# Kernel tuning notes

Measured on AMD Instinct MI355X. Metric: run time of the kernel, lower is better.

The kernel has to match this reference:

```python
import jax, jax.numpy as jnp
import numpy as np

B, C, N = 8, 256, 4096
S = C // 4  # 64
BN_EPS = 1e-5

def setup_inputs() -> dict:
    key = jax.random.key(0)
    ks = jax.random.split(key, 8)
    scale = lambda fan_in: 1.0 / np.sqrt(fan_in)
    x = jax.random.normal(ks[0], (B, C, N), dtype=jnp.float32)
    W_qk = jax.random.normal(ks[1], (S, C), dtype=jnp.float32) * scale(C)
    W_k2c = jax.random.normal(ks[2], (S, C // 2), dtype=jnp.float32) * scale(C // 2)
    W_v = jax.random.normal(ks[3], (C, C), dtype=jnp.float32) * scale(C)
    b_v = jnp.zeros((C,), dtype=jnp.float32)
    W_t = jax.random.normal(ks[4], (C, C), dtype=jnp.float32) * scale(C)
    b_t = jnp.zeros((C,), dtype=jnp.float32)
    bn_gamma = jnp.ones((C,), dtype=jnp.float32)
    bn_beta = jnp.zeros((C,), dtype=jnp.float32)
    bn_mean = jnp.zeros((C,), dtype=jnp.float32)
    bn_var = jnp.ones((C,), dtype=jnp.float32)
    # random.sample(range(C), S): S distinct channel indices
    idx = jax.random.permutation(ks[5], C)[:S].astype(jnp.int32)
    return {"x": x, "W_qk": W_qk, "W_k2c": W_k2c, "W_v": W_v, "b_v": b_v,
            "W_t": W_t, "b_t": b_t, "bn_gamma": bn_gamma, "bn_beta": bn_beta,
            "bn_mean": bn_mean, "bn_var": bn_var, "idx": idx}

def reference(x, W_qk, W_k2c, W_v, b_v, W_t, b_t,
              bn_gamma, bn_beta, bn_mean, bn_var, idx):
    # q = k projection (tied weights), 1x1 conv == channel matmul
    x_q = jnp.einsum('sc,bcn->bns', W_qk, x)            # [B,N,S]
    x_k = jnp.einsum('sc,bcn->bsn', W_qk, x)            # [B,S,N]
    x_k1 = x[:, idx, :]                                  # random channel gather [B,S,N]
    x_k = jnp.concatenate([x_k, x_k1], axis=1)           # [B,C/2,N]
    x_k = jnp.einsum('sh,bhn->bsn', W_k2c, x_k)          # [B,S,N]
    x_k = jax.nn.softmax(x_k, axis=-2)                   # softmax over channel dim
    x_v = jnp.einsum('oc,bcn->bon', W_v, x) + b_v[None, :, None]  # [B,C,N]
    energy = jnp.einsum('bns,bsm->bnm', x_q, x_k)        # [B,N,N]
    attention = jax.nn.softmax(energy, axis=-1)
    attention = attention / (1e-9 + attention.sum(axis=1, keepdims=True))
    x_r = jnp.einsum('bcn,bnm->bcm', x_v, attention)     # [B,C,N]
    x_r = jnp.einsum('oc,bcm->bom', W_t, x_r) + b_t[None, :, None]
    # BatchNorm1d (inference) + ReLU
    inv = bn_gamma / jnp.sqrt(bn_var + BN_EPS)
    x_r = (x_r - bn_mean[None, :, None]) * inv[None, :, None] + bn_beta[None, :, None]
    x_r = jax.nn.relu(x_r)
    return x + x_r
```

## Files before the change

kernel.cpp:

```cpp
#include <hip/hip_runtime.h>
#include <hip/hip_bf16.h>

#define B_ 8
#define C_ 256
#define N_ 4096
#define S_ 64
#define LOG2E 1.4426950408889634f

typedef __attribute__((ext_vector_type(8))) short short8;
typedef __attribute__((ext_vector_type(4))) float f32x4;

__device__ __forceinline__ short f2b(float f) {
  unsigned u = __float_as_uint(f);
  unsigned r = (u + 0x7FFFu + ((u >> 16) & 1u)) >> 16;
  return (short)(r & 0xFFFFu);
}

__device__ __forceinline__ int cvtpk(float lo, float hi) {
  int r;
  asm("v_cvt_pk_bf16_f32 %0, %1, %2" : "=v"(r) : "v"(lo), "v"(hi));
  return r;
}


__global__ __launch_bounds__(256) void kw_conv(const float* __restrict__ Wv,
    const float* __restrict__ Wt, short* __restrict__ Wvf, short* __restrict__ Wtf) {
  int t = blockIdx.x * 256 + threadIdx.x;
  const float* src = (t < 8192) ? Wv : Wt;
  short* dst = (t < 8192) ? Wvf : Wtf;
  int i = (t & 8191) * 8;
  int o = i >> 8, c0c = i & 255;
  short8 v;
#pragma unroll
  for (int j = 0; j < 8; j++) v[j] = f2b(src[i + j]);
  int lane = (o & 15) + 16 * ((c0c >> 3) & 3);
  size_t off = ((((size_t)(o >> 4)) * 8 + (c0c >> 5)) * 64 + lane) * 8;
  *(short8*)(dst + off) = v;
}

__global__ __launch_bounds__(256) void k1_qk(const float* __restrict__ x,
    const float* __restrict__ Wqk, const float* __restrict__ Wk2c,
    const int* __restrict__ idx, short* __restrict__ Qf, short* __restrict__ Kf,
    short* __restrict__ Xf) {
  int bid = blockIdx.x;
  int b = bid & 7, n0 = (bid >> 3) * 64;
  int tn = threadIdx.x;
  int sg = __builtin_amdgcn_readfirstlane(threadIdx.y);
  const float* xb = x + (size_t)b * C_ * N_ + n0 + tn;
  __shared__ short xls[256][73];
  __shared__ float q_lds[64][65];
  __shared__ float red[4][64];
#pragma unroll 4
  for (int i = 0; i < 64; i++) {
    int c = sg * 64 + i;
    xls[c][tn] = f2b(xb[(size_t)c * N_]);
  }
  float acc[16];
#pragma unroll
  for (int i = 0; i < 16; i++) acc[i] = 0.f;
  for (int c = 0; c < C_; c += 4) {
    float x0 = xb[(size_t)c * N_];
    float x1 = xb[(size_t)(c + 1) * N_];
    float x2 = xb[(size_t)(c + 2) * N_];
    float x3 = xb[(size_t)(c + 3) * N_];
#pragma unroll
    for (int i = 0; i < 16; i++) {
      const float* wr = Wqk + (sg * 16 + i) * C_ + c;
      acc[i] += wr[0] * x0 + wr[1] * x1 + wr[2] * x2 + wr[3] * x3;
    }
  }
#pragma unroll
  for (int i = 0; i < 16; i++) q_lds[sg * 16 + i][tn] = acc[i];
  {
    size_t base = (((size_t)b * 256 + (n0 >> 4) + (tn >> 4)) * 2 + (sg >> 1)) * 64;
    int l0 = (tn & 15) + 16 * ((2 * sg) & 3);
    int l1 = (tn & 15) + 16 * ((2 * sg + 1) & 3);
    short8 o0, o1;
#pragma unroll
    for (int i = 0; i < 8; i++) { o0[i] = f2b(acc[i] * LOG2E); o1[i] = f2b(acc[i + 8] * LOG2E); }
    *(short8*)(Qf + (base + l0) * 8) = o0;
    *(short8*)(Qf + (base + l1) * 8) = o1;
  }
  __syncthreads();
#pragma unroll
  for (int i = 0; i < 8; i++) {
    int run = i * 4 + sg;
    int ntl = run >> 3, ks = run & 7;
    short8 o;
#pragma unroll
    for (int j = 0; j < 8; j++)
      o[j] = xls[ks * 32 + ((tn >> 4) & 3) * 8 + j][ntl * 16 + (tn & 15)];
    size_t off = ((((size_t)b * 256 + (n0 >> 4) + ntl) * 8 + ks) * 64 + tn) * 8;
    *(short8*)(Xf + off) = o;
  }
  float acc2[16];
#pragma unroll
  for (int i = 0; i < 16; i++) acc2[i] = 0.f;
  for (int h = 0; h < 64; h += 4) {
    float q0 = q_lds[h][tn], q1 = q_lds[h + 1][tn];
    float q2 = q_lds[h + 2][tn], q3 = q_lds[h + 3][tn];
#pragma unroll
    for (int i = 0; i < 16; i++) {
      const float* wr = Wk2c + (sg * 16 + i) * 128 + h;
      acc2[i] += wr[0] * q0 + wr[1] * q1 + wr[2] * q2 + wr[3] * q3;
    }
  }
  for (int h = 0; h < 64; h += 4) {
    float g0 = xb[(size_t)idx[h] * N_];
    float g1 = xb[(size_t)idx[h + 1] * N_];
    float g2 = xb[(size_t)idx[h + 2] * N_];
    float g3 = xb[(size_t)idx[h + 3] * N_];
#pragma unroll
    for (int i = 0; i < 16; i++) {
      const float* wr = Wk2c + (sg * 16 + i) * 128 + 64 + h;
      acc2[i] += wr[0] * g0 + wr[1] * g1 + wr[2] * g2 + wr[3] * g3;
    }
  }
  float pm = acc2[0];
#pragma unroll
  for (int i = 1; i < 16; i++) pm = fmaxf(pm, acc2[i]);
  red[sg][tn] = pm;
  __syncthreads();
  float mx = fmaxf(fmaxf(red[0][tn], red[1][tn]), fmaxf(red[2][tn], red[3][tn]));
  float ps = 0.f;
  float ex[16];
#pragma unroll
  for (int i = 0; i < 16; i++) { ex[i] = __expf(acc2[i] - mx); ps += ex[i]; }
  __syncthreads();
  red[sg][tn] = ps;
  __syncthreads();
  float inv = 1.f / (red[0][tn] + red[1][tn] + red[2][tn] + red[3][tn]);
  {
    size_t base = (((size_t)b * 256 + (n0 >> 4) + (tn >> 4)) * 2 + (sg >> 1)) * 64;
    int l0 = (tn & 15) + 16 * ((2 * sg) & 3);
    int l1 = (tn & 15) + 16 * ((2 * sg + 1) & 3);
    short8 o0, o1;
#pragma unroll
    for (int i = 0; i < 8; i++) { o0[i] = f2b(ex[i] * inv); o1[i] = f2b(ex[i + 8] * inv); }
    *(short8*)(Kf + (base + l0) * 8) = o0;
    *(short8*)(Kf + (base + l1) * 8) = o1;
  }
}

__global__ __launch_bounds__(256) void k2_xv(const short* __restrict__ Wvf,
    const float* __restrict__ bv, const short* __restrict__ Xf, short* __restrict__ Vf) {
  int bid = blockIdx.x;
  int b = bid & 7, nblk = bid >> 3;
  int lane = threadIdx.x & 63, w = threadIdx.x >> 6;
  int lr = lane & 15, lg = lane >> 4;
  __shared__ short Vt[64][264];
  f32x4 acc[4][4];
#pragma unroll
  for (int i = 0; i < 4; i++)
#pragma unroll
    for (int j = 0; j < 4; j++) acc[i][j] = {0.f, 0.f, 0.f, 0.f};
#pragma unroll 1
  for (int ks = 0; ks < 8; ks++) {
    short8 bfrag[4];
#pragma unroll
    for (int ns = 0; ns < 4; ns++)
      bfrag[ns] = *(const short8*)(Xf + ((((size_t)b * 256 + nblk * 4 + ns) * 8 + ks) * 64 + lane) * 8);
#pragma unroll
    for (int os = 0; os < 4; os++) {
      short8 af = *(const short8*)(Wvf + ((((size_t)(4 * w + os)) * 8 + ks) * 64 + lane) * 8);
#pragma unroll
      for (int ns = 0; ns < 4; ns++)
        acc[os][ns] = __builtin_amdgcn_mfma_f32_16x16x32_bf16(af, bfrag[ns], acc[os][ns], 0, 0, 0);
    }
  }
#pragma unroll
  for (int os = 0; os < 4; os++) {
    int c0 = w * 64 + os * 16 + lg * 4;
    float b0 = bv[c0], b1 = bv[c0 + 1], b2 = bv[c0 + 2], b3 = bv[c0 + 3];
#pragma unroll
    for (int ns = 0; ns < 4; ns++) {
      int2 pk;
      pk.x = cvtpk(acc[os][ns][0] + b0, acc[os][ns][1] + b1);
      pk.y = cvtpk(acc[os][ns][2] + b2, acc[os][ns][3] + b3);
      *(int2*)(&Vt[ns * 16 + lr][c0]) = pk;
    }
  }
  __syncthreads();
#pragma unroll
  for (int rr = 0; rr < 8; rr++) {
    int run = rr * 256 + threadIdx.x;
    int ksl = run >> 10, ctile = (run >> 6) & 15, ln = run & 63;
    short8 o;
#pragma unroll
    for (int j = 0; j < 8; j++)
      o[j] = Vt[ksl * 32 + ((ln >> 4) & 3) * 8 + j][ctile * 16 + (ln & 15)];
    size_t off = ((((size_t)b * 128 + 2 * nblk + ksl) * 16 + ctile) * 64 + ln) * 8;
    *(short8*)(Vf + off) = o;
  }
}

__global__ __launch_bounds__(256) void k3_rse(const short* __restrict__ Qf,
    const short* __restrict__ Kf, float* __restrict__ inv_rse) {
  int bid = blockIdx.x;
  int b = bid & 7, n0 = (bid >> 3) * 64;
  int lane = threadIdx.x & 63, w = threadIdx.x >> 6;
  int lg = lane >> 4;
  const short* Qb = Qf + (size_t)b * 256 * 2 * 512;
  const short* Kb = Kf + (size_t)b * 256 * 2 * 512;
  short8 qf[2];
#pragma unroll
  for (int ks = 0; ks < 2; ks++)
    qf[ks] = *(const short8*)(Qb + ((((size_t)(n0 >> 4) + w) * 2 + ks) * 64 + lane) * 8);
  short8 kc[4][2], kn[4][2];
#pragma unroll
  for (int ms = 0; ms < 4; ms++)
#pragma unroll
    for (int ks = 0; ks < 2; ks++)
      kc[ms][ks] = *(const short8*)(Kb + ((((size_t)ms) * 2 + ks) * 64 + lane) * 8);
  float rs[4] = {0.f, 0.f, 0.f, 0.f};
#pragma unroll 1
  for (int it = 0; it < 64; ++it) {
    int itn = (it < 63) ? it + 1 : it;
#pragma unroll
    for (int ms = 0; ms < 4; ms++)
#pragma unroll
      for (int ks = 0; ks < 2; ks++)
        kn[ms][ks] = *(const short8*)(Kb + ((((size_t)(itn * 4 + ms)) * 2 + ks) * 64 + lane) * 8);
#pragma unroll
    for (int ms = 0; ms < 4; ms++) {
      f32x4 e = {0.f, 0.f, 0.f, 0.f};
#pragma unroll
      for (int ks = 0; ks < 2; ks++)
        e = __builtin_amdgcn_mfma_f32_16x16x32_bf16(qf[ks], kc[ms][ks], e, 0, 0, 0);
#pragma unroll
      for (int r = 0; r < 4; r++) rs[r] += __builtin_amdgcn_exp2f(e[r]);
    }
#pragma unroll
    for (int ms = 0; ms < 4; ms++)
#pragma unroll
      for (int ks = 0; ks < 2; ks++) kc[ms][ks] = kn[ms][ks];
  }
#pragma unroll
  for (int off = 1; off < 16; off <<= 1)
#pragma unroll
    for (int r = 0; r < 4; r++) rs[r] += __shfl_xor(rs[r], off, 64);
  if ((lane & 15) == 0) {
#pragma unroll
    for (int r = 0; r < 4; r++)
      inv_rse[(size_t)b * N_ + n0 + w * 16 + lg * 4 + r] = 1.f / rs[r];
  }
}

__global__ __launch_bounds__(256, 2) void k4_att(const short* __restrict__ Qf,
    const short* __restrict__ Kf, const short* __restrict__ Vf,
    const float* __restrict__ inv_rse, short* __restrict__ Rf) {
  int bid = blockIdx.x;
  int b = bid & 7, mblk = bid >> 3, m0 = mblk * 64;
  int lane = threadIdx.x & 63, w = threadIdx.x >> 6;
  int lr = lane & 15, lg = lane >> 4;
  __shared__ __align__(16) short lds_raw[64 * 264];
  __shared__ float cs_red[4][64];
  short* attf = lds_raw;
  const short* Qb = Qf + (size_t)b * 256 * 2 * 512;
  const short* Kb = Kf + (size_t)b * 256 * 2 * 512;
  const short* Vb = Vf + (size_t)b * 128 * 16 * 512;
  const float* irb = inv_rse + (size_t)b * N_;
  short8 kfrag[4][2];
#pragma unroll
  for (int ms = 0; ms < 4; ms++)
#pragma unroll
    for (int ks = 0; ks < 2; ks++)
      kfrag[ms][ks] = *(const short8*)(Kb + ((((size_t)(mblk * 4 + ms)) * 2 + ks) * 64 + lane) * 8);
  f32x4 P[4][4];
#pragma unroll
  for (int i = 0; i < 4; i++)
#pragma unroll
    for (int j = 0; j < 4; j++) P[i][j] = {0.f, 0.f, 0.f, 0.f};
  float csum[4] = {0.f, 0.f, 0.f, 0.f};
  short8 qf[2][2];
#pragma unroll
  for (int t = 0; t < 2; t++)
#pragma unroll
    for (int ks = 0; ks < 2; ks++)
      qf[t][ks] = *(const short8*)(Qb + ((((size_t)(t * 4 + w)) * 2 + ks) * 64 + lane) * 8);
  int wln = lr + 16 * ((w & 1) * 2 + (lg >> 1));
  int wjo = (lg & 1) * 4;
  int buf = 0;
#pragma unroll 1
  for (int it2 = 0; it2 < 32; ++it2) {
    f32x4 irv[2];
    irv[0] = *(const f32x4*)(irb + it2 * 128 + w * 16 + lg * 4);
    irv[1] = *(const f32x4*)(irb + it2 * 128 + 64 + w * 16 + lg * 4);
    short8 vf[4][4];
#pragma unroll
    for (int kk = 0; kk < 4; kk++)
#pragma unroll
      for (int cs = 0; cs < 4; cs++)
        vf[kk][cs] = *(const short8*)(Vb + ((((size_t)(it2 * 4 + kk)) * 16 + 4 * w + cs) * 64 + lane) * 8);
    f32x4 e[2][4];
#pragma unroll
    for (int t = 0; t < 2; t++)
#pragma unroll
      for (int ms = 0; ms < 4; ms++) {
        f32x4 a = {0.f, 0.f, 0.f, 0.f};
#pragma unroll
        for (int ks = 0; ks < 2; ks++)
          a = __builtin_amdgcn_mfma_f32_16x16x32_bf16(qf[t][ks], kfrag[ms][ks], a, 0, 0, 0);
        e[t][ms] = a;
      }
    int itn = (it2 < 31) ? it2 + 1 : it2;
    short8 qn[2][2];
#pragma unroll
    for (int t = 0; t < 2; t++)
#pragma unroll
      for (int ks = 0; ks < 2; ks++)
        qn[t][ks] = *(const short8*)(Qb + ((((size_t)(itn * 8 + t * 4 + w)) * 2 + ks) * 64 + lane) * 8);
#pragma unroll
    for (int t = 0; t < 2; t++) {
      int kk = t * 2 + (w >> 1);
#pragma unroll
      for (int ms = 0; ms < 4; ms++) {
        float a0 = __builtin_amdgcn_exp2f(e[t][ms][0]) * irv[t][0];
        float a1 = __builtin_amdgcn_exp2f(e[t][ms][1]) * irv[t][1];
        float a2 = __builtin_amdgcn_exp2f(e[t][ms][2]) * irv[t][2];
        float a3 = __builtin_amdgcn_exp2f(e[t][ms][3]) * irv[t][3];
        csum[ms] += (a0 + a1) + (a2 + a3);
        int2 pk;
        pk.x = cvtpk(a0, a1);
        pk.y = cvtpk(a2, a3);
        *(int2*)(attf + (size_t)buf * 8192 + (kk * 4 + ms) * 512 + wln * 8 + wjo) = pk;
      }
    }
    asm volatile("s_waitcnt lgkmcnt(0)" ::: "memory");
    __builtin_amdgcn_s_barrier();
    __builtin_amdgcn_sched_barrier(0);
    __builtin_amdgcn_s_setprio(1);
#pragma unroll
    for (int kk = 0; kk < 4; kk++) {
      short8 bfr[4];
#pragma unroll
      for (int ms = 0; ms < 4; ms++)
        bfr[ms] = *(const short8*)(attf + (size_t)buf * 8192 + (kk * 4 + ms) * 512 + lane * 8);
#pragma unroll
      for (int cs = 0; cs < 4; cs++)
#pragma unroll
        for (int ms = 0; ms < 4; ms++)
          P[cs][ms] = __builtin_amdgcn_mfma_f32_16x16x32_bf16(vf[kk][cs], bfr[ms], P[cs][ms], 0, 0, 0);
    }
    __builtin_amdgcn_s_setprio(0);
#pragma unroll
    for (int t = 0; t < 2; t++)
#pragma unroll
      for (int ks = 0; ks < 2; ks++) qf[t][ks] = qn[t][ks];
    buf ^= 1;
  }
#pragma unroll
  for (int off = 16; off < 64; off <<= 1)
#pragma unroll
    for (int ms = 0; ms < 4; ms++) csum[ms] += __shfl_xor(csum[ms], off, 64);
  if (lg == 0) {
#pragma unroll
    for (int ms = 0; ms < 4; ms++) cs_red[w][ms * 16 + lr] = csum[ms];
  }
  __syncthreads();
  float cinv[4];
#pragma unroll
  for (int ms = 0; ms < 4; ms++) {
    int m = ms * 16 + lr;
    cinv[ms] = 1.f / (1e-9f + cs_red[0][m] + cs_red[1][m] + cs_red[2][m] + cs_red[3][m]);
  }
  short* Rt = lds_raw;
#pragma unroll
  for (int cs = 0; cs < 4; cs++) {
    int c0 = w * 64 + cs * 16 + lg * 4;
#pragma unroll
    for (int ms = 0; ms < 4; ms++) {
      int2 pk;
      pk.x = cvtpk(P[cs][ms][0] * cinv[ms], P[cs][ms][1] * cinv[ms]);
      pk.y = cvtpk(P[cs][ms][2] * cinv[ms], P[cs][ms][3] * cinv[ms]);
      *(int2*)(Rt + (ms * 16 + lr) * 264 + c0) = pk;
    }
  }
  __syncthreads();
#pragma unroll
  for (int rr = 0; rr < 8; rr++) {
    int run = rr * 256 + threadIdx.x;
    int mtl = run >> 9, ksc = (run >> 6) & 7, ln = run & 63;
    short8 o;
#pragma unroll
    for (int j = 0; j < 8; j++)
      o[j] = Rt[(mtl * 16 + (ln & 15)) * 264 + ksc * 32 + ((ln >> 4) & 3) * 8 + j];
    size_t off = ((((size_t)b * 256 + (m0 >> 4) + mtl) * 8 + ksc) * 64 + ln) * 8;
    *(short8*)(Rf + off) = o;
  }
}

__global__ __launch_bounds__(256) void k5_out(const short* __restrict__ Wtf,
    const float* __restrict__ bt, const float* __restrict__ gamma,
    const float* __restrict__ beta, const float* __restrict__ mean,
    const float* __restrict__ var, const short* __restrict__ Rf,
    const float* __restrict__ x, float* __restrict__ out) {
  int bid = blockIdx.x;
  int b = bid & 7, m0 = (bid >> 3) * 64;
  int lane = threadIdx.x & 63, w = threadIdx.x >> 6;
  int lr = lane & 15, lg = lane >> 4;
  f32x4 acc[4][4];
#pragma unroll
  for (int i = 0; i < 4; i++)
#pragma unroll
    for (int j = 0; j < 4; j++) acc[i][j] = {0.f, 0.f, 0.f, 0.f};
#pragma unroll 1
  for (int ks = 0; ks < 8; ks++) {
    short8 bfr[4];
#pragma unroll
    for (int ms = 0; ms < 4; ms++)
      bfr[ms] = *(const short8*)(Rf + ((((size_t)b * 256 + (m0 >> 4) + ms) * 8 + ks) * 64 + lane) * 8);
#pragma unroll
    for (int os = 0; os < 4; os++) {
      short8 af = *(const short8*)(Wtf + ((((size_t)(4 * w + os)) * 8 + ks) * 64 + lane) * 8);
#pragma unroll
      for (int ms = 0; ms < 4; ms++)
        acc[os][ms] = __builtin_amdgcn_mfma_f32_16x16x32_bf16(af, bfr[ms], acc[os][ms], 0, 0, 0);
    }
  }
  const float* xb = x + (size_t)b * C_ * N_ + m0;
  float* ob = out + (size_t)b * C_ * N_ + m0;
#pragma unroll
  for (int os = 0; os < 4; os++)
#pragma unroll
    for (int r = 0; r < 4; r++) {
      int o = w * 64 + os * 16 + lg * 4 + r;
      float bb = bt[o];
      float iv = gamma[o] * rsqrtf(var[o] + 1e-5f);
      float mn = mean[o], be = beta[o];
#pragma unroll
      for (int ms = 0; ms < 4; ms++) {
        int m = ms * 16 + lr;
        float v = (acc[os][ms][r] + bb - mn) * iv + be;
        v = fmaxf(v, 0.f);
        ob[(size_t)o * N_ + m] = xb[(size_t)o * N_ + m] + v;
      }
    }
}

extern "C" void kernel_launch(void* const* d_in, const int* in_sizes, int n_in,
                              void* d_out, int out_size, void* d_ws, size_t ws_size,
                              hipStream_t stream) {
  const float* x     = (const float*)d_in[0];
  const float* Wqk   = (const float*)d_in[1];
  const float* Wk2c  = (const float*)d_in[2];
  const float* Wv    = (const float*)d_in[3];
  const float* bv    = (const float*)d_in[4];
  const float* Wt    = (const float*)d_in[5];
  const float* bt    = (const float*)d_in[6];
  const float* gamma = (const float*)d_in[7];
  const float* beta  = (const float*)d_in[8];
  const float* mean  = (const float*)d_in[9];
  const float* var   = (const float*)d_in[10];
  const int*   idx   = (const int*)d_in[11];
  float* out = (float*)d_out;

  char* ws = (char*)d_ws;
  size_t off = 0;
  auto alloc = [&](size_t bytes) -> void* {
    void* p = ws + off;
    off = (off + bytes + 255) & ~(size_t)255;
    return p;
  };
  short* Xf   = (short*)alloc((size_t)B_ * N_ * C_ * 2);
  short* Qf   = (short*)alloc((size_t)B_ * N_ * S_ * 2);
  short* Kf   = (short*)alloc((size_t)B_ * N_ * S_ * 2);
  short* Vf   = (short*)alloc((size_t)B_ * C_ * N_ * 2);
  float* irse = (float*)alloc((size_t)B_ * N_ * 4);
  short* Rf   = (short*)alloc((size_t)B_ * N_ * C_ * 2);
  short* Wvf  = (short*)alloc((size_t)C_ * C_ * 2);
  short* Wtf  = (short*)alloc((size_t)C_ * C_ * 2);

  kw_conv<<<dim3(64), 256, 0, stream>>>(Wv, Wt, Wvf, Wtf);
  k1_qk<<<dim3(512), dim3(64, 4), 0, stream>>>(x, Wqk, Wk2c, idx, Qf, Kf, Xf);
  k2_xv<<<dim3(512), 256, 0, stream>>>(Wvf, bv, Xf, Vf);
  k3_rse<<<dim3(512), 256, 0, stream>>>(Qf, Kf, irse);
  k4_att<<<dim3(512), 256, 0, stream>>>(Qf, Kf, Vf, irse, Rf);
  k5_out<<<dim3(512), 256, 0, stream>>>(Wtf, bt, gamma, beta, mean, var, Rf, x, out);
}
```

Measured before the change: 337.4 us.

## Fuse output projection into attention kernel and widen blocks to 512 threads

Folds the W_t projection, BatchNorm, ReLU and residual epilogue (the old k5_out) into the attention kernel. The normalized result tile now stays in shared memory instead of going through the Rf global buffer. Both the row-sum kernel and the attention kernel move to 512 threads: eight waves split the key range (k3) or the V k-slices (k4) in two, and the halves are combined through shared memory. This removes one launch and a full bf16 intermediate round trip and doubles the waves per block. The cost is extra shared-memory reductions, more barriers, and per-block recomputation of W_t fragment loads.

```diff
diff --git a/kernel.cpp b/kernel.cpp
--- a/kernel.cpp
+++ b/kernel.cpp
@@ -194,28 +194,32 @@
   }
 }
 
-__global__ __launch_bounds__(256) void k3_rse(const short* __restrict__ Qf,
+__global__ __launch_bounds__(512) void k3_rse(const short* __restrict__ Qf,
     const short* __restrict__ Kf, float* __restrict__ inv_rse) {
   int bid = blockIdx.x;
   int b = bid & 7, n0 = (bid >> 3) * 64;
-  int lane = threadIdx.x & 63, w = threadIdx.x >> 6;
-  int lg = lane >> 4;
+  int tid = threadIdx.x;
+  int lane = tid & 63, w = tid >> 6;
+  int lr = lane & 15, lg = lane >> 4;
+  int wn = w & 3, wm = w >> 2;
+  __shared__ float red[8][16];
   const short* Qb = Qf + (size_t)b * 256 * 2 * 512;
   const short* Kb = Kf + (size_t)b * 256 * 2 * 512;
   short8 qf[2];
 #pragma unroll
   for (int ks = 0; ks < 2; ks++)
-    qf[ks] = *(const short8*)(Qb + ((((size_t)(n0 >> 4) + w) * 2 + ks) * 64 + lane) * 8);
+    qf[ks] = *(const short8*)(Qb + ((((size_t)((n0 >> 4) + wn)) * 2 + ks) * 64 + lane) * 8);
+  int it0 = wm * 32;
   short8 kc[4][2], kn[4][2];
 #pragma unroll
   for (int ms = 0; ms < 4; ms++)
 #pragma unroll
     for (int ks = 0; ks < 2; ks++)
-      kc[ms][ks] = *(const short8*)(Kb + ((((size_t)ms) * 2 + ks) * 64 + lane) * 8);
+      kc[ms][ks] = *(const short8*)(Kb + ((((size_t)(it0 * 4 + ms)) * 2 + ks) * 64 + lane) * 8);
   float rs[4] = {0.f, 0.f, 0.f, 0.f};
 #pragma unroll 1
-  for (int it = 0; it < 64; ++it) {
-    int itn = (it < 63) ? it + 1 : it;
+  for (int it = it0; it < it0 + 32; ++it) {
+    int itn = (it < it0 + 31) ? it + 1 : it;
 #pragma unroll
     for (int ms = 0; ms < 4; ms++)
 #pragma unroll
@@ -239,23 +243,33 @@
   for (int off = 1; off < 16; off <<= 1)
 #pragma unroll
     for (int r = 0; r < 4; r++) rs[r] += __shfl_xor(rs[r], off, 64);
-  if ((lane & 15) == 0) {
-#pragma unroll
-    for (int r = 0; r < 4; r++)
-      inv_rse[(size_t)b * N_ + n0 + w * 16 + lg * 4 + r] = 1.f / rs[r];
-  }
-}
-
-__global__ __launch_bounds__(256, 2) void k4_att(const short* __restrict__ Qf,
+  if (lr == 0) {
+#pragma unroll
+    for (int r = 0; r < 4; r++) red[w][lg * 4 + r] = rs[r];
+  }
+  __syncthreads();
+  if (tid < 64) {
+    int ntl = tid >> 4, i = tid & 15;
+    inv_rse[(size_t)b * N_ + n0 + ntl * 16 + i] = 1.f / (red[ntl][i] + red[ntl + 4][i]);
+  }
+}
+
+__global__ __launch_bounds__(512, 4) void k4_att(const short* __restrict__ Qf,
     const short* __restrict__ Kf, const short* __restrict__ Vf,
-    const float* __restrict__ inv_rse, short* __restrict__ Rf) {
+    const float* __restrict__ inv_rse, const short* __restrict__ Wtf,
+    const float* __restrict__ bt, const float* __restrict__ gamma,
+    const float* __restrict__ beta, const float* __restrict__ mean,
+    const float* __restrict__ var, const float* __restrict__ x,
+    float* __restrict__ out) {
   int bid = blockIdx.x;
   int b = bid & 7, mblk = bid >> 3, m0 = mblk * 64;
-  int lane = threadIdx.x & 63, w = threadIdx.x >> 6;
+  int tid = threadIdx.x;
+  int lane = tid & 63, w = tid >> 6;
   int lr = lane & 15, lg = lane >> 4;
-  __shared__ __align__(16) short lds_raw[64 * 264];
-  __shared__ float cs_red[4][64];
-  short* attf = lds_raw;
+  int wt = w >> 2;
+  int wq = w & 3;
+  __shared__ __align__(16) short attf[2][16][64][8];
+  __shared__ float cs_red[8][64];
   const short* Qb = Qf + (size_t)b * 256 * 2 * 512;
   const short* Kb = Kf + (size_t)b * 256 * 2 * 512;
   const short* Vb = Vf + (size_t)b * 128 * 16 * 512;
@@ -272,81 +286,67 @@
 #pragma unroll
     for (int j = 0; j < 4; j++) P[i][j] = {0.f, 0.f, 0.f, 0.f};
   float csum[4] = {0.f, 0.f, 0.f, 0.f};
-  short8 qf[2][2];
-#pragma unroll
-  for (int t = 0; t < 2; t++)
-#pragma unroll
-    for (int ks = 0; ks < 2; ks++)
-      qf[t][ks] = *(const short8*)(Qb + ((((size_t)(t * 4 + w)) * 2 + ks) * 64 + lane) * 8);
-  int wln = lr + 16 * ((w & 1) * 2 + (lg >> 1));
+  short8 qf[2];
+#pragma unroll
+  for (int ks = 0; ks < 2; ks++)
+    qf[ks] = *(const short8*)(Qb + ((((size_t)w) * 2 + ks) * 64 + lane) * 8);
+  int kkw = w >> 1;
+  int wln = lr + 16 * (((w & 1) << 1) | (lg >> 1));
   int wjo = (lg & 1) * 4;
   int buf = 0;
 #pragma unroll 1
   for (int it2 = 0; it2 < 32; ++it2) {
-    f32x4 irv[2];
-    irv[0] = *(const f32x4*)(irb + it2 * 128 + w * 16 + lg * 4);
-    irv[1] = *(const f32x4*)(irb + it2 * 128 + 64 + w * 16 + lg * 4);
-    short8 vf[4][4];
-#pragma unroll
-    for (int kk = 0; kk < 4; kk++)
+    f32x4 irv = *(const f32x4*)(irb + it2 * 128 + w * 16 + lg * 4);
+    short8 vf[2][4];
+#pragma unroll
+    for (int kkl = 0; kkl < 2; kkl++)
 #pragma unroll
       for (int cs = 0; cs < 4; cs++)
-        vf[kk][cs] = *(const short8*)(Vb + ((((size_t)(it2 * 4 + kk)) * 16 + 4 * w + cs) * 64 + lane) * 8);
-    f32x4 e[2][4];
-#pragma unroll
-    for (int t = 0; t < 2; t++)
-#pragma unroll
-      for (int ms = 0; ms < 4; ms++) {
-        f32x4 a = {0.f, 0.f, 0.f, 0.f};
-#pragma unroll
-        for (int ks = 0; ks < 2; ks++)
-          a = __builtin_amdgcn_mfma_f32_16x16x32_bf16(qf[t][ks], kfrag[ms][ks], a, 0, 0, 0);
-        e[t][ms] = a;
-      }
+        vf[kkl][cs] = *(const short8*)(Vb + ((((size_t)(it2 * 4 + wt * 2 + kkl)) * 16 + wq * 4 + cs) * 64 + lane) * 8);
+    f32x4 e[4];
+#pragma unroll
+    for (int ms = 0; ms < 4; ms++) {
+      f32x4 a = {0.f, 0.f, 0.f, 0.f};
+#pragma unroll
+      for (int ks = 0; ks < 2; ks++)
+        a = __builtin_amdgcn_mfma_f32_16x16x32_bf16(qf[ks], kfrag[ms][ks], a, 0, 0, 0);
+      e[ms] = a;
+    }
     int itn = (it2 < 31) ? it2 + 1 : it2;
-    short8 qn[2][2];
-#pragma unroll
-    for (int t = 0; t < 2; t++)
-#pragma unroll
-      for (int ks = 0; ks < 2; ks++)
-        qn[t][ks] = *(const short8*)(Qb + ((((size_t)(itn * 8 + t * 4 + w)) * 2 + ks) * 64 + lane) * 8);
-#pragma unroll
-    for (int t = 0; t < 2; t++) {
-      int kk = t * 2 + (w >> 1);
-#pragma unroll
-      for (int ms = 0; ms < 4; ms++) {
-        float a0 = __builtin_amdgcn_exp2f(e[t][ms][0]) * irv[t][0];
-        float a1 = __builtin_amdgcn_exp2f(e[t][ms][1]) * irv[t][1];
-        float a2 = __builtin_amdgcn_exp2f(e[t][ms][2]) * irv[t][2];
-        float a3 = __builtin_amdgcn_exp2f(e[t][ms][3]) * irv[t][3];
-        csum[ms] += (a0 + a1) + (a2 + a3);
-        int2 pk;
-        pk.x = cvtpk(a0, a1);
-        pk.y = cvtpk(a2, a3);
-        *(int2*)(attf + (size_t)buf * 8192 + (kk * 4 + ms) * 512 + wln * 8 + wjo) = pk;
-      }
-    }
-    asm volatile("s_waitcnt lgkmcnt(0)" ::: "memory");
-    __builtin_amdgcn_s_barrier();
-    __builtin_amdgcn_sched_barrier(0);
+    short8 qn[2];
+#pragma unroll
+    for (int ks = 0; ks < 2; ks++)
+      qn[ks] = *(const short8*)(Qb + ((((size_t)(itn * 8 + w)) * 2 + ks) * 64 + lane) * 8);
+#pragma unroll
+    for (int ms = 0; ms < 4; ms++) {
+      float a0 = __builtin_amdgcn_exp2f(e[ms][0]) * irv[0];
+      float a1 = __builtin_amdgcn_exp2f(e[ms][1]) * irv[1];
+      float a2 = __builtin_amdgcn_exp2f(e[ms][2]) * irv[2];
+      float a3 = __builtin_amdgcn_exp2f(e[ms][3]) * irv[3];
+      csum[ms] += (a0 + a1) + (a2 + a3);
+      int2 pk;
+      pk.x = cvtpk(a0, a1);
+      pk.y = cvtpk(a2, a3);
+      *(int2*)(&attf[buf][kkw * 4 + ms][wln][wjo]) = pk;
+    }
+    __syncthreads();
     __builtin_amdgcn_s_setprio(1);
 #pragma unroll
-    for (int kk = 0; kk < 4; kk++) {
+    for (int kkl = 0; kkl < 2; kkl++) {
+      int kkg = wt * 2 + kkl;
       short8 bfr[4];
 #pragma unroll
       for (int ms = 0; ms < 4; ms++)
-        bfr[ms] = *(const short8*)(attf + (size_t)buf * 8192 + (kk * 4 + ms) * 512 + lane * 8);
+        bfr[ms] = *(const short8*)(&attf[buf][kkg * 4 + ms][lane][0]);
 #pragma unroll
       for (int cs = 0; cs < 4; cs++)
 #pragma unroll
         for (int ms = 0; ms < 4; ms++)
-          P[cs][ms] = __builtin_amdgcn_mfma_f32_16x16x32_bf16(vf[kk][cs], bfr[ms], P[cs][ms], 0, 0, 0);
+          P[cs][ms] = __builtin_amdgcn_mfma_f32_16x16x32_bf16(vf[kkl][cs], bfr[ms], P[cs][ms], 0, 0, 0);
     }
     __builtin_amdgcn_s_setprio(0);
 #pragma unroll
-    for (int t = 0; t < 2; t++)
-#pragma unroll
-      for (int ks = 0; ks < 2; ks++) qf[t][ks] = qn[t][ks];
+    for (int ks = 0; ks < 2; ks++) qf[ks] = qn[ks];
     buf ^= 1;
   }
 #pragma unroll
@@ -362,76 +362,78 @@
 #pragma unroll
   for (int ms = 0; ms < 4; ms++) {
     int m = ms * 16 + lr;
-    cinv[ms] = 1.f / (1e-9f + cs_red[0][m] + cs_red[1][m] + cs_red[2][m] + cs_red[3][m]);
-  }
-  short* Rt = lds_raw;
-#pragma unroll
+    float s = 0.f;
+#pragma unroll
+    for (int ww = 0; ww < 8; ww++) s += cs_red[ww][m];
+    cinv[ms] = 1.f / (1e-9f + s);
+  }
+  float* Pex = (float*)&attf[0][0][0][0];
+#pragma unroll 1
   for (int cs = 0; cs < 4; cs++) {
-    int c0 = w * 64 + cs * 16 + lg * 4;
-#pragma unroll
-    for (int ms = 0; ms < 4; ms++) {
-      int2 pk;
-      pk.x = cvtpk(P[cs][ms][0] * cinv[ms], P[cs][ms][1] * cinv[ms]);
-      pk.y = cvtpk(P[cs][ms][2] * cinv[ms], P[cs][ms][3] * cinv[ms]);
-      *(int2*)(Rt + (ms * 16 + lr) * 264 + c0) = pk;
-    }
-  }
-  __syncthreads();
-#pragma unroll
-  for (int rr = 0; rr < 8; rr++) {
-    int run = rr * 256 + threadIdx.x;
-    int mtl = run >> 9, ksc = (run >> 6) & 7, ln = run & 63;
-    short8 o;
-#pragma unroll
-    for (int j = 0; j < 8; j++)
-      o[j] = Rt[(mtl * 16 + (ln & 15)) * 264 + ksc * 32 + ((ln >> 4) & 3) * 8 + j];
-    size_t off = ((((size_t)b * 256 + (m0 >> 4) + mtl) * 8 + ksc) * 64 + ln) * 8;
-    *(short8*)(Rf + off) = o;
-  }
-}
-
-__global__ __launch_bounds__(256) void k5_out(const short* __restrict__ Wtf,
-    const float* __restrict__ bt, const float* __restrict__ gamma,
-    const float* __restrict__ beta, const float* __restrict__ mean,
-    const float* __restrict__ var, const short* __restrict__ Rf,
-    const float* __restrict__ x, float* __restrict__ out) {
-  int bid = blockIdx.x;
-  int b = bid & 7, m0 = (bid >> 3) * 64;
-  int lane = threadIdx.x & 63, w = threadIdx.x >> 6;
-  int lr = lane & 15, lg = lane >> 4;
-  f32x4 acc[4][4];
-#pragma unroll
-  for (int i = 0; i < 4; i++)
-#pragma unroll
-    for (int j = 0; j < 4; j++) acc[i][j] = {0.f, 0.f, 0.f, 0.f};
+    if (wt == 1) {
+#pragma unroll
+      for (int ms = 0; ms < 4; ms++)
+        *(f32x4*)(Pex + ((wq * 4 + ms) * 64 + lane) * 4) = P[cs][ms];
+    }
+    __syncthreads();
+    if (wt == 0) {
+#pragma unroll
+      for (int ms = 0; ms < 4; ms++) {
+        f32x4 t = *(const f32x4*)(Pex + ((wq * 4 + ms) * 64 + lane) * 4);
+        P[cs][ms] += t;
+      }
+    }
+    __syncthreads();
+  }
+  short* Rt = (short*)&attf[0][0][0][0];
+  if (wt == 0) {
+#pragma unroll
+    for (int cs = 0; cs < 4; cs++) {
+      int ks = wq * 2 + (cs >> 1);
+      int lt = lr + 16 * (((cs & 1) << 1) | (lg >> 1));
+#pragma unroll
+      for (int ms = 0; ms < 4; ms++) {
+        int2 pk;
+        pk.x = cvtpk(P[cs][ms][0] * cinv[ms], P[cs][ms][1] * cinv[ms]);
+        pk.y = cvtpk(P[cs][ms][2] * cinv[ms], P[cs][ms][3] * cinv[ms]);
+        *(int2*)(Rt + ((ms * 8 + ks) * 512 + lt * 8 + (lg & 1) * 4)) = pk;
+      }
+    }
+  }
+  __syncthreads();
+  f32x4 acc2[2][4];
+#pragma unroll
+  for (int i = 0; i < 2; i++)
+#pragma unroll
+    for (int j = 0; j < 4; j++) acc2[i][j] = {0.f, 0.f, 0.f, 0.f};
 #pragma unroll 1
   for (int ks = 0; ks < 8; ks++) {
-    short8 bfr[4];
+    short8 bfr2[4];
 #pragma unroll
     for (int ms = 0; ms < 4; ms++)
-      bfr[ms] = *(const short8*)(Rf + ((((size_t)b * 256 + (m0 >> 4) + ms) * 8 + ks) * 64 + lane) * 8);
-#pragma unroll
-    for (int os = 0; os < 4; os++) {
-      short8 af = *(const short8*)(Wtf + ((((size_t)(4 * w + os)) * 8 + ks) * 64 + lane) * 8);
+      bfr2[ms] = *(const short8*)(Rt + ((ms * 8 + ks) * 512 + lane * 8));
+#pragma unroll
+    for (int os = 0; os < 2; os++) {
+      short8 af = *(const short8*)(Wtf + ((((size_t)(w * 2 + os)) * 8 + ks) * 64 + lane) * 8);
 #pragma unroll
       for (int ms = 0; ms < 4; ms++)
-        acc[os][ms] = __builtin_amdgcn_mfma_f32_16x16x32_bf16(af, bfr[ms], acc[os][ms], 0, 0, 0);
+        acc2[os][ms] = __builtin_amdgcn_mfma_f32_16x16x32_bf16(af, bfr2[ms], acc2[os][ms], 0, 0, 0);
     }
   }
   const float* xb = x + (size_t)b * C_ * N_ + m0;
   float* ob = out + (size_t)b * C_ * N_ + m0;
 #pragma unroll
-  for (int os = 0; os < 4; os++)
+  for (int os = 0; os < 2; os++)
 #pragma unroll
     for (int r = 0; r < 4; r++) {
-      int o = w * 64 + os * 16 + lg * 4 + r;
+      int o = w * 32 + os * 16 + lg * 4 + r;
       float bb = bt[o];
       float iv = gamma[o] * rsqrtf(var[o] + 1e-5f);
       float mn = mean[o], be = beta[o];
 #pragma unroll
       for (int ms = 0; ms < 4; ms++) {
         int m = ms * 16 + lr;
-        float v = (acc[os][ms][r] + bb - mn) * iv + be;
+        float v = (acc2[os][ms][r] + bb - mn) * iv + be;
         v = fmaxf(v, 0.f);
         ob[(size_t)o * N_ + m] = xb[(size_t)o * N_ + m] + v;
       }
@@ -467,14 +469,13 @@
   short* Kf   = (short*)alloc((size_t)B_ * N_ * S_ * 2);
   short* Vf   = (short*)alloc((size_t)B_ * C_ * N_ * 2);
   float* irse = (float*)alloc((size_t)B_ * N_ * 4);
-  short* Rf   = (short*)alloc((size_t)B_ * N_ * C_ * 2);
   short* Wvf  = (short*)alloc((size_t)C_ * C_ * 2);
   short* Wtf  = (short*)alloc((size_t)C_ * C_ * 2);
 
   kw_conv<<<dim3(64), 256, 0, stream>>>(Wv, Wt, Wvf, Wtf);
   k1_qk<<<dim3(512), dim3(64, 4), 0, stream>>>(x, Wqk, Wk2c, idx, Qf, Kf, Xf);
   k2_xv<<<dim3(512), 256, 0, stream>>>(Wvf, bv, Xf, Vf);
-  k3_rse<<<dim3(512), 256, 0, stream>>>(Qf, Kf, irse);
-  k4_att<<<dim3(512), 256, 0, stream>>>(Qf, Kf, Vf, irse, Rf);
-  k5_out<<<dim3(512), 256, 0, stream>>>(Wtf, bt, gamma, beta, mean, var, Rf, x, out);
-}
+  k3_rse<<<dim3(512), 512, 0, stream>>>(Qf, Kf, irse);
+  k4_att<<<dim3(512), 512, 0, stream>>>(Qf, Kf, Vf, irse, Wtf,
+                                        bt, gamma, beta, mean, var, x, out);
+}
```

Result: slower. 1.125 ms (+233.4%).
